# Performance work log

Hardware: AMD Instinct MI355X
Metric: run time of the kernel (lower is better)

Reference implementation:

```python
import jax, jax.numpy as jnp
import numpy as np

NUM_GROUPS = 32
EPS = 1e-5


def group_norm(x, gamma, beta):
    # x: [B, C, H, W]; normalize per group of C//NUM_GROUPS channels over (c_in_group, H, W)
    B, C, H, W = x.shape
    xg = x.reshape(B, NUM_GROUPS, C // NUM_GROUPS, H, W)
    mean = jnp.mean(xg, axis=(2, 3, 4), keepdims=True)
    var = jnp.var(xg, axis=(2, 3, 4), keepdims=True)
    xn = ((xg - mean) * jax.lax.rsqrt(var + EPS)).reshape(B, C, H, W)
    return xn * gamma[None, :, None, None] + beta[None, :, None, None]


def setup_inputs() -> dict:
    key = jax.random.key(0)
    kx, kq, kp = jax.random.split(key, 3)
    B, C, H, W = 4, 256, 64, 64
    x = jax.random.normal(kx, (B, C, H, W), dtype=jnp.float32)
    gamma = jnp.ones((C,), dtype=jnp.float32)
    beta = jnp.zeros((C,), dtype=jnp.float32)
    # 1x1 convs == channel matmuls; weights [out_c, in_c]
    w_qkv = jax.random.normal(kq, (3 * C, C), dtype=jnp.float32) / np.sqrt(C)
    w_proj = jax.random.normal(kp, (C, C), dtype=jnp.float32) / np.sqrt(C)
    return {"x": x, "t": 0, "gamma": gamma, "beta": beta, "w_qkv": w_qkv, "w_proj": w_proj}


def reference(x, t, gamma, beta, w_qkv, w_proj):
    B, C, H, W = x.shape
    normed = group_norm(x, gamma, beta)  # [B,C,H,W]
    qkv = jnp.einsum('bchw,oc->bohw', normed, w_qkv)  # [B,3C,H,W]
    q, k, v = jnp.split(qkv, 3, axis=1)
    N = H * W
    q = q.reshape(B, C, N)
    k = k.reshape(B, C, N)
    v = v.reshape(B, C, N)
    # scores[b,i,j] = sum_c q[b,c,i] k[b,c,j] / sqrt(C)
    scores = jnp.einsum('bci,bcj->bij', q, k) / jnp.sqrt(jnp.asarray(C, x.dtype))
    attn = jax.nn.softmax(scores, axis=-1)  # [B,N,N]
    # out[b,c,i] = sum_j v[b,c,j] attn[b,i,j]
    out = jnp.einsum('bcj,bij->bci', v, attn).reshape(B, C, H, W)
    out = jnp.einsum('bchw,oc->bohw', out, w_proj)
    return x + out
```

## Files before the change

### kernel.cpp

```cpp
#include <hip/hip_runtime.h>

typedef __bf16 bf16x8 __attribute__((ext_vector_type(8)));
typedef float floatx4 __attribute__((ext_vector_type(4)));
typedef float floatx16 __attribute__((ext_vector_type(16)));
typedef unsigned int u32;

#define BB 4
#define CC 256
#define NN 4096

__device__ __forceinline__ unsigned short f2bf(float f) {
  union { float f; unsigned u; } v; v.f = f;
  unsigned r = v.u + 0x7fffu + ((v.u >> 16) & 1u);
  return (unsigned short)(r >> 16);
}

__device__ __forceinline__ float bf2f(unsigned short s) {
  union { unsigned u; float f; } v; v.u = ((u32)s) << 16;
  return v.f;
}

__device__ __forceinline__ void async16(const void* g, void* l) {
  __builtin_amdgcn_global_load_lds((const __attribute__((address_space(1))) u32*)g,
                                   (__attribute__((address_space(3))) u32*)l, 16, 0, 0);
}

__device__ __forceinline__ u32 fbits(float f) {
  union { float f; u32 u; } v; v.f = f; return v.u;
}

__global__ __launch_bounds__(256) void gn_stats(const float* __restrict__ x, float* __restrict__ mr) {
  int bg = blockIdx.x;
  const float* p = x + (size_t)bg * 32768;
  int t = threadIdx.x;
  float s = 0.f, q = 0.f;
#pragma unroll
  for (int it = 0; it < 32; ++it) {
    float4 v = *(const float4*)(p + it * 1024 + t * 4);
    s += v.x + v.y + v.z + v.w;
    q += v.x * v.x + v.y * v.y + v.z * v.z + v.w * v.w;
  }
#pragma unroll
  for (int off = 1; off < 64; off <<= 1) {
    s += __shfl_xor(s, off, 64);
    q += __shfl_xor(q, off, 64);
  }
  __shared__ float red[8];
  int w = t >> 6;
  if ((t & 63) == 0) { red[w] = s; red[4 + w] = q; }
  __syncthreads();
  if (t == 0) {
    float S = red[0] + red[1] + red[2] + red[3];
    float Q = red[4] + red[5] + red[6] + red[7];
    float mean = S * (1.f / 32768.f);
    float var = Q * (1.f / 32768.f) - mean * mean;
    mr[bg] = mean;
    mr[128 + bg] = rsqrtf(var + 1e-5f);
  }
}

__global__ __launch_bounds__(256) void gn_apply(const float* __restrict__ x, const float* __restrict__ mr,
                                                const float* __restrict__ gamma, const float* __restrict__ beta,
                                                unsigned short* __restrict__ normed) {
  int bid = blockIdx.x;
  int nt = bid & 63;
  int ct = (bid >> 6) & 3;
  int b = bid >> 8;
  int c0 = ct * 64, n0 = nt * 64;
  __shared__ unsigned short T[64][80];
  int t = threadIdx.x;
#pragma unroll
  for (int it = 0; it < 4; ++it) {
    int idx = it * 256 + t;
    int cl = idx >> 4;
    int n4 = (idx & 15) * 4;
    int c = c0 + cl;
    int bg = b * 32 + (c >> 3);
    float mean = mr[bg], rstd = mr[128 + bg];
    float sc = rstd * gamma[c];
    float sh = beta[c] - mean * sc;
    float4 v = *(const float4*)(x + ((size_t)(b * CC + c)) * NN + n0 + n4);
    T[n4 + 0][cl] = f2bf(v.x * sc + sh);
    T[n4 + 1][cl] = f2bf(v.y * sc + sh);
    T[n4 + 2][cl] = f2bf(v.z * sc + sh);
    T[n4 + 3][cl] = f2bf(v.w * sc + sh);
  }
  __syncthreads();
#pragma unroll
  for (int it = 0; it < 2; ++it) {
    int idx = it * 256 + t;
    int nl = idx >> 3, ck = idx & 7;
    uint4 val;
    unsigned short* pv = (unsigned short*)&val;
#pragma unroll
    for (int j = 0; j < 8; ++j) pv[j] = T[nl][ck * 8 + j];
    *(uint4*)(normed + ((size_t)b * NN + n0 + nl) * CC + c0 + ck * 8) = val;
  }
}

__global__ __launch_bounds__(256) void wconv(const float* __restrict__ wqkv, const float* __restrict__ wproj,
                                             unsigned short* __restrict__ wq_bf, unsigned short* __restrict__ wp_bf) {
  int i = blockIdx.x * 256 + threadIdx.x;
  if (i < 196608) {
    float v = wqkv[i];
    if (i < 65536) v *= 0.090168440055560213f;
    wq_bf[i] = f2bf(v);
  } else {
    int j = i - 196608;
    wp_bf[j] = f2bf(wproj[j]);
  }
}

template <int RESID>
__global__ __launch_bounds__(256) void gemm_bt(const unsigned short* __restrict__ A,
                                               const unsigned short* __restrict__ Bm,
                                               void* __restrict__ Cout, const float* __restrict__ resid,
                                               int mtiles, int ldc,
                                               long sA, long sB, long sC, long sR) {
  int mt = blockIdx.x % mtiles;
  int nt = blockIdx.x / mtiles;
  int b = blockIdx.y;
  int m0 = mt * 128, n0 = nt * 128;
  __shared__ unsigned short As[128][72];
  __shared__ unsigned short Bs[128][72];
  int t = threadIdx.x;
  int w = t >> 6, lane = t & 63;
  int l16 = lane & 15, quad = lane >> 4;
  int wr = w >> 1, wc = w & 1;
  const unsigned short* Ab = A + (size_t)b * sA + (size_t)m0 * 256;
  const unsigned short* Bb = Bm + (size_t)b * sB + (size_t)n0 * 256;
  floatx4 acc[4][4];
#pragma unroll
  for (int m = 0; m < 4; ++m)
#pragma unroll
    for (int n = 0; n < 4; ++n)
#pragma unroll
      for (int r = 0; r < 4; ++r) acc[m][n][r] = 0.f;

  for (int kb = 0; kb < 4; ++kb) {
    __syncthreads();
#pragma unroll
    for (int i = 0; i < 4; ++i) {
      int idx = i * 256 + t;
      int r = idx >> 3, ck = idx & 7;
      *(uint4*)&As[r][ck * 8] = *(const uint4*)(Ab + (size_t)r * 256 + kb * 64 + ck * 8);
      *(uint4*)&Bs[r][ck * 8] = *(const uint4*)(Bb + (size_t)r * 256 + kb * 64 + ck * 8);
    }
    __syncthreads();
#pragma unroll
    for (int kk = 0; kk < 2; ++kk) {
      bf16x8 af[4], bfr[4];
#pragma unroll
      for (int m = 0; m < 4; ++m) af[m] = *(const bf16x8*)&As[wr * 64 + m * 16 + l16][kk * 32 + quad * 8];
#pragma unroll
      for (int n = 0; n < 4; ++n) bfr[n] = *(const bf16x8*)&Bs[wc * 64 + n * 16 + l16][kk * 32 + quad * 8];
#pragma unroll
      for (int m = 0; m < 4; ++m)
#pragma unroll
        for (int n = 0; n < 4; ++n)
          acc[m][n] = __builtin_amdgcn_mfma_f32_16x16x32_bf16(af[m], bfr[n], acc[m][n], 0, 0, 0);
    }
  }
  size_t cb = (size_t)b * sC;
  size_t rb = (size_t)b * sR;
#pragma unroll
  for (int m = 0; m < 4; ++m)
#pragma unroll
    for (int n = 0; n < 4; ++n)
#pragma unroll
      for (int r = 0; r < 4; ++r) {
        int row = m0 + wr * 64 + m * 16 + quad * 4 + r;
        int col = n0 + wc * 64 + n * 16 + l16;
        size_t idx = (size_t)row * ldc + col;
        if (RESID)
          ((float*)Cout)[cb + idx] = acc[m][n][r] + resid[rb + idx];
        else
          ((unsigned short*)Cout)[cb + idx] = f2bf(acc[m][n][r]);
      }
}

__global__ __launch_bounds__(512, 2) void attn(const unsigned short* __restrict__ qk,
                                               const unsigned short* __restrict__ vbuf,
                                               unsigned short* __restrict__ opart0,
                                               unsigned short* __restrict__ opart1,
                                               float* __restrict__ lpart) {
  __shared__ __attribute__((aligned(16))) char smem[131072];

  int xcd = blockIdx.x & 7, slot = blockIdx.x >> 3;
  int b = xcd >> 1;
  int kh = xcd & 1;
  int i0 = slot * 128;
  int k0 = kh * 32;

  int t = threadIdx.x, w = t >> 6, l = t & 63;
  int l31 = l & 31, hi = l >> 5;
  int iq = w & 3;
  int ch = w >> 2;

  const size_t bqk = (size_t)b * NN * 512;
  const size_t bv = (size_t)b * CC * NN;

  auto stage = [&](int tile, int buf) {
    const unsigned short* kg = qk + bqk + (size_t)tile * 64 * 512 + 256;
    char* kb = smem + buf * 32768;
#pragma unroll
    for (int it = 0; it < 4; ++it) {
      int pp = w * 4 + it;
      int r = 2 * pp + (l >> 5);
      int c = (l & 31) ^ (r & 31);
      async16(kg + (size_t)r * 512 + c * 8, kb + pp * 1024);
    }
    const unsigned short* vg = vbuf + bv + (size_t)tile * 64;
    char* vb = smem + 65536 + buf * 32768;
    int cj = (l & 7) ^ ((l >> 3) & 7);
#pragma unroll
    for (int it = 0; it < 4; ++it) {
      int pp = w * 4 + it;
      int rc = 8 * pp + (l >> 3);
      async16(vg + (size_t)rc * NN + cj * 8, vb + pp * 1024);
    }
  };

  stage(k0, 0);

  bf16x8 qreg[16];
  {
    const unsigned short* qp = qk + bqk + (size_t)(i0 + iq * 32 + l31) * 512 + hi * 8;
#pragma unroll
    for (int ks = 0; ks < 16; ++ks)
      qreg[ks] = *(const bf16x8*)(qp + ks * 16);
  }

  floatx16 oacc[4];
#pragma unroll
  for (int cf = 0; cf < 4; ++cf)
#pragma unroll
    for (int r = 0; r < 16; ++r) oacc[cf][r] = 0.f;
  float lacc = 0.f;

  for (int kt = 0; kt < 32; ++kt) {
    int cur = kt & 1;
    __syncthreads();
    if (kt < 31) stage(k0 + kt + 1, cur ^ 1);

    const unsigned short* Kc = (const unsigned short*)(smem + cur * 32768);
    const unsigned short* Vc = (const unsigned short*)(smem + 65536 + cur * 32768);

#pragma unroll
    for (int jh = 0; jh < 2; ++jh) {
      floatx16 st;
#pragma unroll
      for (int r = 0; r < 16; ++r) st[r] = 0.f;
#pragma unroll
      for (int ks = 0; ks < 16; ++ks) {
        bf16x8 kf = *(const bf16x8*)&Kc[(jh * 32 + l31) * 256 + (((ks << 1) | hi) ^ l31) * 8];
        st = __builtin_amdgcn_mfma_f32_32x32x16_bf16(kf, qreg[ks], st, 0, 0, 0);
      }
      u32 pr[8];
#pragma unroll
      for (int k2 = 0; k2 < 8; ++k2) {
        float p0 = __builtin_amdgcn_exp2f(st[2 * k2]);
        float p1 = __builtin_amdgcn_exp2f(st[2 * k2 + 1]);
        lacc += p0 + p1;
        pr[k2] = __builtin_amdgcn_perm(fbits(p1), fbits(p0), 0x07060302u);
      }
      union U { u32 u[4]; bf16x8 v; } a0, a1;
      {
        u32 sA = hi ? pr[0] : pr[2], sB = hi ? pr[1] : pr[3];
        u32 rA = (u32)__shfl_xor((int)sA, 32, 64);
        u32 rB = (u32)__shfl_xor((int)sB, 32, 64);
        a0.u[0] = hi ? rA : pr[0]; a0.u[1] = hi ? rB : pr[1];
        a0.u[2] = hi ? pr[2] : rA; a0.u[3] = hi ? pr[3] : rB;
        sA = hi ? pr[4] : pr[6]; sB = hi ? pr[5] : pr[7];
        rA = (u32)__shfl_xor((int)sA, 32, 64);
        rB = (u32)__shfl_xor((int)sB, 32, 64);
        a1.u[0] = hi ? rA : pr[4]; a1.u[1] = hi ? rB : pr[5];
        a1.u[2] = hi ? pr[6] : rA; a1.u[3] = hi ? pr[7] : rB;
      }
#pragma unroll
      for (int cf = 0; cf < 4; ++cf) {
        int c = ch * 128 + cf * 32 + l31;
        const unsigned short* vrow = Vc + c * 64;
        bf16x8 v0 = *(const bf16x8*)(vrow + (((jh * 4) | hi) ^ (l31 & 7)) * 8);
        oacc[cf] = __builtin_amdgcn_mfma_f32_32x32x16_bf16(a0.v, v0, oacc[cf], 0, 0, 0);
        bf16x8 v1 = *(const bf16x8*)(vrow + (((jh * 4 + 2) | hi) ^ (l31 & 7)) * 8);
        oacc[cf] = __builtin_amdgcn_mfma_f32_32x32x16_bf16(a1.v, v1, oacc[cf], 0, 0, 0);
      }
    }
  }

  float l2 = lacc + __shfl_xor(lacc, 32, 64);
  size_t pbl = (size_t)(b * 2 + kh) * NN + i0;
  if (ch == 0 && hi == 0) lpart[pbl + iq * 32 + l31] = l2;

  unsigned short* ops = kh ? opart1 : opart0;
  size_t rowbase = (size_t)b * NN + i0 + iq * 32;
#pragma unroll
  for (int cf = 0; cf < 4; ++cf)
#pragma unroll
    for (int r = 0; r < 16; ++r) {
      int il = (r & 3) + 8 * (r >> 2) + 4 * hi;
      ops[(rowbase + il) * CC + ch * 128 + cf * 32 + l31] = f2bf(oacc[cf][r]);
    }
}

__global__ __launch_bounds__(256) void attn_combine(const unsigned short* __restrict__ op0,
                                                    const unsigned short* __restrict__ op1,
                                                    const float* __restrict__ lp,
                                                    unsigned short* __restrict__ obuf) {
  int gid = blockIdx.x * 256 + threadIdx.x;
  int e = gid * 8;
  int b = e >> 20;
  int inner = e & 1048575;
  int n = inner >> 8;
  float linv = 1.f / (lp[b * 8192 + n] + lp[b * 8192 + 4096 + n]);
  size_t off = (size_t)b * 1048576 + inner;
  uint4 u0 = *(const uint4*)(op0 + off);
  uint4 u1 = *(const uint4*)(op1 + off);
  const unsigned short* a = (const unsigned short*)&u0;
  const unsigned short* c = (const unsigned short*)&u1;
  union { unsigned short us[8]; uint4 q; } o;
#pragma unroll
  for (int j = 0; j < 8; ++j)
    o.us[j] = f2bf((bf2f(a[j]) + bf2f(c[j])) * linv);
  *(uint4*)(obuf + e) = o.q;
}

extern "C" void kernel_launch(void* const* d_in, const int* in_sizes, int n_in,
                              void* d_out, int out_size, void* d_ws, size_t ws_size,
                              hipStream_t stream) {
  const float* x     = (const float*)d_in[0];
  const float* gamma = (const float*)d_in[2];
  const float* beta  = (const float*)d_in[3];
  const float* wqkv  = (const float*)d_in[4];
  const float* wproj = (const float*)d_in[5];
  float* out = (float*)d_out;

  char* p = (char*)d_ws;
  float* mr               = (float*)(p + 0);
  unsigned short* wq_bf   = (unsigned short*)(p + 1024);
  unsigned short* wp_bf   = (unsigned short*)(p + 394240);
  unsigned short* normed  = (unsigned short*)(p + 525312);
  unsigned short* qkbuf   = (unsigned short*)(p + 8913920);
  unsigned short* vbuf    = (unsigned short*)(p + 25691136);
  unsigned short* opart1  = (unsigned short*)(p + 34079744);
  unsigned short* opart0  = normed;
  float* lpart            = (float*)(p + 1024);
  unsigned short* obuf    = qkbuf;
  unsigned short* wv_bf   = wq_bf + 512 * 256;

  wconv<<<1024, 256, 0, stream>>>(wqkv, wproj, wq_bf, wp_bf);
  gn_stats<<<128, 256, 0, stream>>>(x, mr);
  gn_apply<<<1024, 256, 0, stream>>>(x, mr, gamma, beta, normed);
  gemm_bt<0><<<dim3(128, 4), 256, 0, stream>>>(normed, wq_bf, qkbuf, nullptr,
                                               32, 512, (long)NN * CC, 0L, (long)NN * 512, 0L);
  gemm_bt<0><<<dim3(64, 4), 256, 0, stream>>>(wv_bf, normed, vbuf, nullptr,
                                              2, 4096, 0L, (long)NN * CC, (long)CC * NN, 0L);
  attn<<<256, 512, 0, stream>>>(qkbuf, vbuf, opart0, opart1, lpart);
  attn_combine<<<2048, 256, 0, stream>>>(opart0, opart1, lpart, obuf);
  gemm_bt<1><<<dim3(64, 4), 256, 0, stream>>>(wp_bf, obuf, out, x,
                                              2, 4096, 0L, (long)NN * CC, (long)CC * NN, (long)CC * NN);
}
```

Measured before the change: 213.4 us.

## Halve attention block to 4 waves, each computing two 32-row query tiles

The attention kernel drops from 8 waves to 4 waves per block, and each wave now handles two 32-query sub-tiles. Each K fragment read from LDS feeds two QK MFMAs and each V fragment feeds two PV MFMAs, which halves LDS read traffic per unit of math. In exchange, register pressure roughly doubles (two Q register sets and eight output accumulators), fewer waves are available to hide latency, and each thread issues twice as many async staging loads.

```diff
diff --git a/kernel.cpp b/kernel.cpp
--- a/kernel.cpp
+++ b/kernel.cpp
@@ -179,7 +179,7 @@
       }
 }
 
-__global__ __launch_bounds__(512, 2) void attn(const unsigned short* __restrict__ qk,
+__global__ __launch_bounds__(256, 1) void attn(const unsigned short* __restrict__ qk,
                                                const unsigned short* __restrict__ vbuf,
                                                unsigned short* __restrict__ opart0,
                                                unsigned short* __restrict__ opart1,
@@ -194,8 +194,8 @@
 
   int t = threadIdx.x, w = t >> 6, l = t & 63;
   int l31 = l & 31, hi = l >> 5;
-  int iq = w & 3;
-  int ch = w >> 2;
+  int ih = w & 1;
+  int ch = w >> 1;
 
   const size_t bqk = (size_t)b * NN * 512;
   const size_t bv = (size_t)b * CC * NN;
@@ -204,8 +204,8 @@
     const unsigned short* kg = qk + bqk + (size_t)tile * 64 * 512 + 256;
     char* kb = smem + buf * 32768;
 #pragma unroll
-    for (int it = 0; it < 4; ++it) {
-      int pp = w * 4 + it;
+    for (int it = 0; it < 8; ++it) {
+      int pp = w * 8 + it;
       int r = 2 * pp + (l >> 5);
       int c = (l & 31) ^ (r & 31);
       async16(kg + (size_t)r * 512 + c * 8, kb + pp * 1024);
@@ -214,8 +214,8 @@
     char* vb = smem + 65536 + buf * 32768;
     int cj = (l & 7) ^ ((l >> 3) & 7);
 #pragma unroll
-    for (int it = 0; it < 4; ++it) {
-      int pp = w * 4 + it;
+    for (int it = 0; it < 8; ++it) {
+      int pp = w * 8 + it;
       int rc = 8 * pp + (l >> 3);
       async16(vg + (size_t)rc * NN + cj * 8, vb + pp * 1024);
     }
@@ -223,20 +223,23 @@
 
   stage(k0, 0);
 
-  bf16x8 qreg[16];
-  {
-    const unsigned short* qp = qk + bqk + (size_t)(i0 + iq * 32 + l31) * 512 + hi * 8;
+  bf16x8 qreg[2][16];
+#pragma unroll
+  for (int ib = 0; ib < 2; ++ib) {
+    const unsigned short* qp = qk + bqk + (size_t)(i0 + ih * 64 + ib * 32 + l31) * 512 + hi * 8;
 #pragma unroll
     for (int ks = 0; ks < 16; ++ks)
-      qreg[ks] = *(const bf16x8*)(qp + ks * 16);
-  }
-
-  floatx16 oacc[4];
-#pragma unroll
-  for (int cf = 0; cf < 4; ++cf)
-#pragma unroll
-    for (int r = 0; r < 16; ++r) oacc[cf][r] = 0.f;
-  float lacc = 0.f;
+      qreg[ib][ks] = *(const bf16x8*)(qp + ks * 16);
+  }
+
+  floatx16 oacc[2][4];
+#pragma unroll
+  for (int ib = 0; ib < 2; ++ib)
+#pragma unroll
+    for (int cf = 0; cf < 4; ++cf)
+#pragma unroll
+      for (int r = 0; r < 16; ++r) oacc[ib][cf][r] = 0.f;
+  float lacc0 = 0.f, lacc1 = 0.f;
 
   for (int kt = 0; kt < 32; ++kt) {
     int cur = kt & 1;
@@ -248,60 +251,75 @@
 
 #pragma unroll
     for (int jh = 0; jh < 2; ++jh) {
-      floatx16 st;
-#pragma unroll
-      for (int r = 0; r < 16; ++r) st[r] = 0.f;
+      floatx16 st0, st1;
+#pragma unroll
+      for (int r = 0; r < 16; ++r) { st0[r] = 0.f; st1[r] = 0.f; }
 #pragma unroll
       for (int ks = 0; ks < 16; ++ks) {
         bf16x8 kf = *(const bf16x8*)&Kc[(jh * 32 + l31) * 256 + (((ks << 1) | hi) ^ l31) * 8];
-        st = __builtin_amdgcn_mfma_f32_32x32x16_bf16(kf, qreg[ks], st, 0, 0, 0);
-      }
-      u32 pr[8];
+        st0 = __builtin_amdgcn_mfma_f32_32x32x16_bf16(kf, qreg[0][ks], st0, 0, 0, 0);
+        st1 = __builtin_amdgcn_mfma_f32_32x32x16_bf16(kf, qreg[1][ks], st1, 0, 0, 0);
+      }
+      u32 pr0[8], pr1[8];
 #pragma unroll
       for (int k2 = 0; k2 < 8; ++k2) {
-        float p0 = __builtin_amdgcn_exp2f(st[2 * k2]);
-        float p1 = __builtin_amdgcn_exp2f(st[2 * k2 + 1]);
-        lacc += p0 + p1;
-        pr[k2] = __builtin_amdgcn_perm(fbits(p1), fbits(p0), 0x07060302u);
-      }
-      union U { u32 u[4]; bf16x8 v; } a0, a1;
-      {
+        float a0 = __builtin_amdgcn_exp2f(st0[2 * k2]);
+        float a1 = __builtin_amdgcn_exp2f(st0[2 * k2 + 1]);
+        lacc0 += a0 + a1;
+        pr0[k2] = __builtin_amdgcn_perm(fbits(a1), fbits(a0), 0x07060302u);
+        float b0 = __builtin_amdgcn_exp2f(st1[2 * k2]);
+        float b1 = __builtin_amdgcn_exp2f(st1[2 * k2 + 1]);
+        lacc1 += b0 + b1;
+        pr1[k2] = __builtin_amdgcn_perm(fbits(b1), fbits(b0), 0x07060302u);
+      }
+      union U { u32 u[4]; bf16x8 v; } a0[2], a1[2];
+#pragma unroll
+      for (int ib = 0; ib < 2; ++ib) {
+        u32* pr = ib ? pr1 : pr0;
         u32 sA = hi ? pr[0] : pr[2], sB = hi ? pr[1] : pr[3];
         u32 rA = (u32)__shfl_xor((int)sA, 32, 64);
         u32 rB = (u32)__shfl_xor((int)sB, 32, 64);
-        a0.u[0] = hi ? rA : pr[0]; a0.u[1] = hi ? rB : pr[1];
-        a0.u[2] = hi ? pr[2] : rA; a0.u[3] = hi ? pr[3] : rB;
+        a0[ib].u[0] = hi ? rA : pr[0]; a0[ib].u[1] = hi ? rB : pr[1];
+        a0[ib].u[2] = hi ? pr[2] : rA; a0[ib].u[3] = hi ? pr[3] : rB;
         sA = hi ? pr[4] : pr[6]; sB = hi ? pr[5] : pr[7];
         rA = (u32)__shfl_xor((int)sA, 32, 64);
         rB = (u32)__shfl_xor((int)sB, 32, 64);
-        a1.u[0] = hi ? rA : pr[4]; a1.u[1] = hi ? rB : pr[5];
-        a1.u[2] = hi ? pr[6] : rA; a1.u[3] = hi ? pr[7] : rB;
+        a1[ib].u[0] = hi ? rA : pr[4]; a1[ib].u[1] = hi ? rB : pr[5];
+        a1[ib].u[2] = hi ? pr[6] : rA; a1[ib].u[3] = hi ? pr[7] : rB;
       }
 #pragma unroll
       for (int cf = 0; cf < 4; ++cf) {
         int c = ch * 128 + cf * 32 + l31;
         const unsigned short* vrow = Vc + c * 64;
         bf16x8 v0 = *(const bf16x8*)(vrow + (((jh * 4) | hi) ^ (l31 & 7)) * 8);
-        oacc[cf] = __builtin_amdgcn_mfma_f32_32x32x16_bf16(a0.v, v0, oacc[cf], 0, 0, 0);
+        oacc[0][cf] = __builtin_amdgcn_mfma_f32_32x32x16_bf16(a0[0].v, v0, oacc[0][cf], 0, 0, 0);
+        oacc[1][cf] = __builtin_amdgcn_mfma_f32_32x32x16_bf16(a0[1].v, v0, oacc[1][cf], 0, 0, 0);
         bf16x8 v1 = *(const bf16x8*)(vrow + (((jh * 4 + 2) | hi) ^ (l31 & 7)) * 8);
-        oacc[cf] = __builtin_amdgcn_mfma_f32_32x32x16_bf16(a1.v, v1, oacc[cf], 0, 0, 0);
-      }
-    }
-  }
-
-  float l2 = lacc + __shfl_xor(lacc, 32, 64);
+        oacc[0][cf] = __builtin_amdgcn_mfma_f32_32x32x16_bf16(a1[0].v, v1, oacc[0][cf], 0, 0, 0);
+        oacc[1][cf] = __builtin_amdgcn_mfma_f32_32x32x16_bf16(a1[1].v, v1, oacc[1][cf], 0, 0, 0);
+      }
+    }
+  }
+
+  float l20 = lacc0 + __shfl_xor(lacc0, 32, 64);
+  float l21 = lacc1 + __shfl_xor(lacc1, 32, 64);
   size_t pbl = (size_t)(b * 2 + kh) * NN + i0;
-  if (ch == 0 && hi == 0) lpart[pbl + iq * 32 + l31] = l2;
+  if (ch == 0 && hi == 0) {
+    lpart[pbl + ih * 64 + l31] = l20;
+    lpart[pbl + ih * 64 + 32 + l31] = l21;
+  }
 
   unsigned short* ops = kh ? opart1 : opart0;
-  size_t rowbase = (size_t)b * NN + i0 + iq * 32;
-#pragma unroll
-  for (int cf = 0; cf < 4; ++cf)
-#pragma unroll
-    for (int r = 0; r < 16; ++r) {
-      int il = (r & 3) + 8 * (r >> 2) + 4 * hi;
-      ops[(rowbase + il) * CC + ch * 128 + cf * 32 + l31] = f2bf(oacc[cf][r]);
-    }
+  size_t rowbase = (size_t)b * NN + i0 + ih * 64;
+#pragma unroll
+  for (int ib = 0; ib < 2; ++ib)
+#pragma unroll
+    for (int cf = 0; cf < 4; ++cf)
+#pragma unroll
+      for (int r = 0; r < 16; ++r) {
+        int il = (r & 3) + 8 * (r >> 2) + 4 * hi;
+        ops[(rowbase + ib * 32 + il) * CC + ch * 128 + cf * 32 + l31] = f2bf(oacc[ib][cf][r]);
+      }
 }
 
 __global__ __launch_bounds__(256) void attn_combine(const unsigned short* __restrict__ op0,
@@ -356,7 +374,7 @@
                                                32, 512, (long)NN * CC, 0L, (long)NN * 512, 0L);
   gemm_bt<0><<<dim3(64, 4), 256, 0, stream>>>(wv_bf, normed, vbuf, nullptr,
                                               2, 4096, 0L, (long)NN * CC, (long)CC * NN, 0L);
-  attn<<<256, 512, 0, stream>>>(qkbuf, vbuf, opart0, opart1, lpart);
+  attn<<<256, 256, 0, stream>>>(qkbuf, vbuf, opart0, opart1, lpart);
   attn_combine<<<2048, 256, 0, stream>>>(opart0, opart1, lpart, obuf);
   gemm_bt<1><<<dim3(64, 4), 256, 0, stream>>>(wp_bf, obuf, out, x,
                                               2, 4096, 0L, (long)NN * CC, (long)CC * NN, (long)CC * NN);
```

Measured after the change: 229.4 us. 7.5% more time.

## Split attention waves by key half and fuse combine into projection GEMM

Applied to the files above, without the earlier changes.

Attention waves now each own one 32-key half of a tile and all 256 channels, instead of splitting channels and each computing scores for both key halves. This removes the duplicated QK^T MFMAs across channel groups. The two key-half partial outputs and row sums are then reduced through shared memory at the end. The separate combine kernel is removed: a new projection GEMM sums the two split-K partials and applies 1/l while loading its B tile. This trades extra accumulator registers and an LDS reduction for less matrix work and one fewer launch and memory pass.

```diff
diff --git a/kernel.cpp b/kernel.cpp
--- a/kernel.cpp
+++ b/kernel.cpp
@@ -194,8 +194,8 @@
 
   int t = threadIdx.x, w = t >> 6, l = t & 63;
   int l31 = l & 31, hi = l >> 5;
-  int iq = w & 3;
-  int ch = w >> 2;
+  int jh = w & 1;
+  int iq = w >> 1;
 
   const size_t bqk = (size_t)b * NN * 512;
   const size_t bv = (size_t)b * CC * NN;
@@ -231,9 +231,9 @@
       qreg[ks] = *(const bf16x8*)(qp + ks * 16);
   }
 
-  floatx16 oacc[4];
-#pragma unroll
-  for (int cf = 0; cf < 4; ++cf)
+  floatx16 oacc[8];
+#pragma unroll
+  for (int cf = 0; cf < 8; ++cf)
 #pragma unroll
     for (int r = 0; r < 16; ++r) oacc[cf][r] = 0.f;
   float lacc = 0.f;
@@ -246,84 +246,157 @@
     const unsigned short* Kc = (const unsigned short*)(smem + cur * 32768);
     const unsigned short* Vc = (const unsigned short*)(smem + 65536 + cur * 32768);
 
-#pragma unroll
-    for (int jh = 0; jh < 2; ++jh) {
-      floatx16 st;
-#pragma unroll
-      for (int r = 0; r < 16; ++r) st[r] = 0.f;
-#pragma unroll
-      for (int ks = 0; ks < 16; ++ks) {
-        bf16x8 kf = *(const bf16x8*)&Kc[(jh * 32 + l31) * 256 + (((ks << 1) | hi) ^ l31) * 8];
-        st = __builtin_amdgcn_mfma_f32_32x32x16_bf16(kf, qreg[ks], st, 0, 0, 0);
+    floatx16 st;
+#pragma unroll
+    for (int r = 0; r < 16; ++r) st[r] = 0.f;
+#pragma unroll
+    for (int ks = 0; ks < 16; ++ks) {
+      bf16x8 kf = *(const bf16x8*)&Kc[(jh * 32 + l31) * 256 + (((ks << 1) | hi) ^ l31) * 8];
+      st = __builtin_amdgcn_mfma_f32_32x32x16_bf16(kf, qreg[ks], st, 0, 0, 0);
+    }
+
+    u32 pr[8];
+#pragma unroll
+    for (int k2 = 0; k2 < 8; ++k2) {
+      float p0 = __builtin_amdgcn_exp2f(st[2 * k2]);
+      float p1 = __builtin_amdgcn_exp2f(st[2 * k2 + 1]);
+      lacc += p0 + p1;
+      pr[k2] = __builtin_amdgcn_perm(fbits(p1), fbits(p0), 0x07060302u);
+    }
+
+    union U { u32 u[4]; bf16x8 v; } a0, a1;
+    {
+      u32 sA = hi ? pr[0] : pr[2], sB = hi ? pr[1] : pr[3];
+      u32 rA = (u32)__shfl_xor((int)sA, 32, 64);
+      u32 rB = (u32)__shfl_xor((int)sB, 32, 64);
+      a0.u[0] = hi ? rA : pr[0]; a0.u[1] = hi ? rB : pr[1];
+      a0.u[2] = hi ? pr[2] : rA; a0.u[3] = hi ? pr[3] : rB;
+      sA = hi ? pr[4] : pr[6]; sB = hi ? pr[5] : pr[7];
+      rA = (u32)__shfl_xor((int)sA, 32, 64);
+      rB = (u32)__shfl_xor((int)sB, 32, 64);
+      a1.u[0] = hi ? rA : pr[4]; a1.u[1] = hi ? rB : pr[5];
+      a1.u[2] = hi ? pr[6] : rA; a1.u[3] = hi ? pr[7] : rB;
+    }
+
+#pragma unroll
+    for (int cf = 0; cf < 8; ++cf) {
+      const unsigned short* vrow = Vc + (cf * 32 + l31) * 64;
+      bf16x8 v0 = *(const bf16x8*)(vrow + (((jh * 4) | hi) ^ (l31 & 7)) * 8);
+      oacc[cf] = __builtin_amdgcn_mfma_f32_32x32x16_bf16(a0.v, v0, oacc[cf], 0, 0, 0);
+      bf16x8 v1 = *(const bf16x8*)(vrow + (((jh * 4 + 2) | hi) ^ (l31 & 7)) * 8);
+      oacc[cf] = __builtin_amdgcn_mfma_f32_32x32x16_bf16(a1.v, v1, oacc[cf], 0, 0, 0);
+    }
+  }
+
+  float l2 = lacc + __shfl_xor(lacc, 32, 64);
+
+  float* Of = (float*)smem + iq * 8192;
+  __syncthreads();
+  if (jh == 1) {
+#pragma unroll
+    for (int cf = 0; cf < 8; ++cf)
+#pragma unroll
+      for (int r = 0; r < 16; ++r) {
+        int il = (r & 3) + 8 * (r >> 2) + 4 * hi;
+        Of[il * 256 + cf * 32 + l31] = oacc[cf][r];
       }
-      u32 pr[8];
-#pragma unroll
-      for (int k2 = 0; k2 < 8; ++k2) {
-        float p0 = __builtin_amdgcn_exp2f(st[2 * k2]);
-        float p1 = __builtin_amdgcn_exp2f(st[2 * k2 + 1]);
-        lacc += p0 + p1;
-        pr[k2] = __builtin_amdgcn_perm(fbits(p1), fbits(p0), 0x07060302u);
-      }
-      union U { u32 u[4]; bf16x8 v; } a0, a1;
-      {
-        u32 sA = hi ? pr[0] : pr[2], sB = hi ? pr[1] : pr[3];
-        u32 rA = (u32)__shfl_xor((int)sA, 32, 64);
-        u32 rB = (u32)__shfl_xor((int)sB, 32, 64);
-        a0.u[0] = hi ? rA : pr[0]; a0.u[1] = hi ? rB : pr[1];
-        a0.u[2] = hi ? pr[2] : rA; a0.u[3] = hi ? pr[3] : rB;
-        sA = hi ? pr[4] : pr[6]; sB = hi ? pr[5] : pr[7];
-        rA = (u32)__shfl_xor((int)sA, 32, 64);
-        rB = (u32)__shfl_xor((int)sB, 32, 64);
-        a1.u[0] = hi ? rA : pr[4]; a1.u[1] = hi ? rB : pr[5];
-        a1.u[2] = hi ? pr[6] : rA; a1.u[3] = hi ? pr[7] : rB;
-      }
-#pragma unroll
-      for (int cf = 0; cf < 4; ++cf) {
-        int c = ch * 128 + cf * 32 + l31;
-        const unsigned short* vrow = Vc + c * 64;
-        bf16x8 v0 = *(const bf16x8*)(vrow + (((jh * 4) | hi) ^ (l31 & 7)) * 8);
-        oacc[cf] = __builtin_amdgcn_mfma_f32_32x32x16_bf16(a0.v, v0, oacc[cf], 0, 0, 0);
-        bf16x8 v1 = *(const bf16x8*)(vrow + (((jh * 4 + 2) | hi) ^ (l31 & 7)) * 8);
-        oacc[cf] = __builtin_amdgcn_mfma_f32_32x32x16_bf16(a1.v, v1, oacc[cf], 0, 0, 0);
-      }
-    }
-  }
-
-  float l2 = lacc + __shfl_xor(lacc, 32, 64);
-  size_t pbl = (size_t)(b * 2 + kh) * NN + i0;
-  if (ch == 0 && hi == 0) lpart[pbl + iq * 32 + l31] = l2;
-
+  }
+  __syncthreads();
   unsigned short* ops = kh ? opart1 : opart0;
   size_t rowbase = (size_t)b * NN + i0 + iq * 32;
-#pragma unroll
-  for (int cf = 0; cf < 4; ++cf)
-#pragma unroll
-    for (int r = 0; r < 16; ++r) {
-      int il = (r & 3) + 8 * (r >> 2) + 4 * hi;
-      ops[(rowbase + il) * CC + ch * 128 + cf * 32 + l31] = f2bf(oacc[cf][r]);
-    }
-}
-
-__global__ __launch_bounds__(256) void attn_combine(const unsigned short* __restrict__ op0,
-                                                    const unsigned short* __restrict__ op1,
-                                                    const float* __restrict__ lp,
-                                                    unsigned short* __restrict__ obuf) {
-  int gid = blockIdx.x * 256 + threadIdx.x;
-  int e = gid * 8;
-  int b = e >> 20;
-  int inner = e & 1048575;
-  int n = inner >> 8;
-  float linv = 1.f / (lp[b * 8192 + n] + lp[b * 8192 + 4096 + n]);
-  size_t off = (size_t)b * 1048576 + inner;
-  uint4 u0 = *(const uint4*)(op0 + off);
-  uint4 u1 = *(const uint4*)(op1 + off);
-  const unsigned short* a = (const unsigned short*)&u0;
-  const unsigned short* c = (const unsigned short*)&u1;
-  union { unsigned short us[8]; uint4 q; } o;
-#pragma unroll
-  for (int j = 0; j < 8; ++j)
-    o.us[j] = f2bf((bf2f(a[j]) + bf2f(c[j])) * linv);
-  *(uint4*)(obuf + e) = o.q;
+  if (jh == 0) {
+#pragma unroll
+    for (int cf = 0; cf < 8; ++cf)
+#pragma unroll
+      for (int r = 0; r < 16; ++r) {
+        int il = (r & 3) + 8 * (r >> 2) + 4 * hi;
+        float v = oacc[cf][r] + Of[il * 256 + cf * 32 + l31];
+        ops[(rowbase + il) * CC + cf * 32 + l31] = f2bf(v);
+      }
+  }
+  __syncthreads();
+  float* Lred = (float*)smem;
+  if (hi == 0) Lred[w * 32 + l31] = l2;
+  __syncthreads();
+  if (jh == 0 && hi == 0) {
+    size_t pbl = (size_t)(b * 2 + kh) * NN + i0;
+    lpart[pbl + iq * 32 + l31] = Lred[(iq * 2) * 32 + l31] + Lred[(iq * 2 + 1) * 32 + l31];
+  }
+}
+
+__global__ __launch_bounds__(256) void gemm_proj(const unsigned short* __restrict__ wp,
+                                                 const unsigned short* __restrict__ op0,
+                                                 const unsigned short* __restrict__ op1,
+                                                 const float* __restrict__ lp,
+                                                 float* __restrict__ out, const float* __restrict__ x) {
+  int mt = blockIdx.x & 1;
+  int nt = blockIdx.x >> 1;
+  int b = blockIdx.y;
+  int m0 = mt * 128, n0 = nt * 128;
+  __shared__ unsigned short As[128][72];
+  __shared__ unsigned short Bs[128][72];
+  __shared__ float Linv[128];
+  int t = threadIdx.x;
+  int w = t >> 6, lane = t & 63;
+  int l16 = lane & 15, quad = lane >> 4;
+  int wr = w >> 1, wc = w & 1;
+  const unsigned short* Ab = wp + (size_t)m0 * 256;
+  const unsigned short* o0 = op0 + ((size_t)b * NN + n0) * 256;
+  const unsigned short* o1 = op1 + ((size_t)b * NN + n0) * 256;
+  if (t < 128) Linv[t] = 1.f / (lp[b * 8192 + n0 + t] + lp[b * 8192 + 4096 + n0 + t]);
+  floatx4 acc[4][4];
+#pragma unroll
+  for (int m = 0; m < 4; ++m)
+#pragma unroll
+    for (int n = 0; n < 4; ++n)
+#pragma unroll
+      for (int r = 0; r < 4; ++r) acc[m][n][r] = 0.f;
+
+  for (int kb = 0; kb < 4; ++kb) {
+    __syncthreads();
+#pragma unroll
+    for (int i = 0; i < 4; ++i) {
+      int idx = i * 256 + t;
+      int r = idx >> 3, ck = idx & 7;
+      *(uint4*)&As[r][ck * 8] = *(const uint4*)(Ab + (size_t)r * 256 + kb * 64 + ck * 8);
+      uint4 u0 = *(const uint4*)(o0 + (size_t)r * 256 + kb * 64 + ck * 8);
+      uint4 u1 = *(const uint4*)(o1 + (size_t)r * 256 + kb * 64 + ck * 8);
+      float li = Linv[r];
+      const unsigned short* pa = (const unsigned short*)&u0;
+      const unsigned short* pb = (const unsigned short*)&u1;
+      union { unsigned short us[8]; uint4 q; } ob;
+#pragma unroll
+      for (int j = 0; j < 8; ++j)
+        ob.us[j] = f2bf((bf2f(pa[j]) + bf2f(pb[j])) * li);
+      *(uint4*)&Bs[r][ck * 8] = ob.q;
+    }
+    __syncthreads();
+#pragma unroll
+    for (int kk = 0; kk < 2; ++kk) {
+      bf16x8 af[4], bfr[4];
+#pragma unroll
+      for (int m = 0; m < 4; ++m) af[m] = *(const bf16x8*)&As[wr * 64 + m * 16 + l16][kk * 32 + quad * 8];
+#pragma unroll
+      for (int n = 0; n < 4; ++n) bfr[n] = *(const bf16x8*)&Bs[wc * 64 + n * 16 + l16][kk * 32 + quad * 8];
+#pragma unroll
+      for (int m = 0; m < 4; ++m)
+#pragma unroll
+        for (int n = 0; n < 4; ++n)
+          acc[m][n] = __builtin_amdgcn_mfma_f32_16x16x32_bf16(af[m], bfr[n], acc[m][n], 0, 0, 0);
+    }
+  }
+  size_t cb = (size_t)b * CC * NN;
+#pragma unroll
+  for (int m = 0; m < 4; ++m)
+#pragma unroll
+    for (int n = 0; n < 4; ++n)
+#pragma unroll
+      for (int r = 0; r < 4; ++r) {
+        int row = m0 + wr * 64 + m * 16 + quad * 4 + r;
+        int col = n0 + wc * 64 + n * 16 + l16;
+        size_t idx = cb + (size_t)row * NN + col;
+        out[idx] = acc[m][n][r] + x[idx];
+      }
 }
 
 extern "C" void kernel_launch(void* const* d_in, const int* in_sizes, int n_in,
@@ -346,7 +419,6 @@
   unsigned short* opart1  = (unsigned short*)(p + 34079744);
   unsigned short* opart0  = normed;
   float* lpart            = (float*)(p + 1024);
-  unsigned short* obuf    = qkbuf;
   unsigned short* wv_bf   = wq_bf + 512 * 256;
 
   wconv<<<1024, 256, 0, stream>>>(wqkv, wproj, wq_bf, wp_bf);
@@ -357,7 +429,5 @@
   gemm_bt<0><<<dim3(64, 4), 256, 0, stream>>>(wv_bf, normed, vbuf, nullptr,
                                               2, 4096, 0L, (long)NN * CC, (long)CC * NN, 0L);
   attn<<<256, 512, 0, stream>>>(qkbuf, vbuf, opart0, opart1, lpart);
-  attn_combine<<<2048, 256, 0, stream>>>(opart0, opart1, lpart, obuf);
-  gemm_bt<1><<<dim3(64, 4), 256, 0, stream>>>(wp_bf, obuf, out, x,
-                                              2, 4096, 0L, (long)NN * CC, (long)CC * NN, (long)CC * NN);
-}
+  gemm_proj<<<dim3(64, 4), 256, 0, stream>>>(wp_bf, opart0, opart1, lpart, out, x);
+}
```

New measurement: 194.8 us. 8.7% less time.
